# Performance work log

Measured on AMD Instinct MI355X. Metric: run time of the kernel, lower is better.

The kernel has to match this reference:

```python
import jax, jax.numpy as jnp
import numpy as np

HEAD_NUM = 8
DIM_QK = 64
DIM_V = 64
SPAN = 64
STRIDE = 4


def _sparse_indices(length_q, length_kv):
    # Replicates torch meshgrid index math (static, numpy).
    R = SPAN // STRIDE
    r = np.arange(R)[:, None]              # [R,1]
    c = np.arange(length_q)[None, :]       # [1,Lq]
    # ceil((c-(span-1))/stride) + r, via floor-div identity ceil(a/b) = -((-a)//b)
    qi_col = -((SPAN - 1 - c) // STRIDE) + r   # [R,Lq]
    qi_row = c - STRIDE * qi_col
    valid = (qi_row >= 0) & (qi_row < SPAN) & (qi_col >= 0) & (qi_col < length_kv)
    qc = np.clip(qi_col, 0, length_kv - 1)
    return jnp.asarray(qc, dtype=jnp.int32), jnp.asarray(valid)


def setup_inputs() -> dict:
    key = jax.random.key(0)
    ks = jax.random.split(key, 7)
    B, Lq, Lkv, D = 2, 4096, 1024, 512
    q = jax.random.normal(ks[0], (B, Lq, D), dtype=jnp.float32)
    k = jax.random.normal(ks[1], (B, Lkv, D), dtype=jnp.float32)
    v = jax.random.normal(ks[2], (B, Lkv, D), dtype=jnp.float32)
    Wq = jax.random.normal(ks[3], (D, HEAD_NUM * DIM_QK), dtype=jnp.float32) * 0.05
    Wk = jax.random.normal(ks[4], (D, HEAD_NUM * DIM_QK), dtype=jnp.float32) * 0.05
    Wv = jax.random.normal(ks[5], (D, HEAD_NUM * DIM_V), dtype=jnp.float32) * 0.05
    Wout = jax.random.normal(ks[6], (HEAD_NUM * DIM_V, D), dtype=jnp.float32) * 0.05
    return {"q": q, "k": k, "v": v, "Wq": Wq, "Wk": Wk, "Wv": Wv, "Wout": Wout}


def reference(q, k, v, Wq, Wk, Wv, Wout):
    B, Lq, _ = q.shape
    Lkv = k.shape[1]
    # Projections -> [B, H, L, D]
    Q = (q @ Wq).reshape(B, Lq, HEAD_NUM, DIM_QK).transpose(0, 2, 1, 3)
    K = (k @ Wk).reshape(B, Lkv, HEAD_NUM, DIM_QK).transpose(0, 2, 1, 3)
    V = (v @ Wv).reshape(B, Lkv, HEAD_NUM, DIM_V).transpose(0, 2, 1, 3)
    qc, valid = _sparse_indices(Lq, Lkv)          # [R,Lq]
    Kg = K[:, :, qc, :]                            # [B,H,R,Lq,DQK] gather
    scores = jnp.einsum("bhcd,bhrcd->bhrc", Q, Kg) / jnp.sqrt(jnp.float32(DIM_QK))
    big_neg = jnp.asarray(-1e30, scores.dtype)
    scores = jnp.where(valid[None, None], scores, big_neg)
    w = jax.nn.softmax(scores, axis=2)             # softmax over the R sparse slots
    w = jnp.where(valid[None, None], w, 0.0)
    Vg = V[:, :, qc, :]                            # [B,H,R,Lq,DV] gather
    ctx = jnp.einsum("bhrc,bhrcd->bhcd", w, Vg)   # [B,H,Lq,DV]
    ctx = ctx.transpose(0, 2, 1, 3).reshape(B, Lq, HEAD_NUM * DIM_V)
    return ctx @ Wout
```

## Files before the change

### kernel.cpp

```cpp
#include <hip/hip_runtime.h>
#include <math.h>

#define HN 8
#define DK 64
#define LQ 4096
#define LKV 1024
#define DMODEL 512
#define BATCH 2

typedef unsigned short u16;
typedef unsigned int u32;
typedef __attribute__((ext_vector_type(8))) __bf16 bf16x8;
typedef __attribute__((ext_vector_type(4))) float f32x4;
typedef __attribute__((ext_vector_type(8))) u16 u16x8;

__device__ __forceinline__ u16 f2bf(float f) {
    u32 u = __float_as_uint(f);
    u = u + 0x7fffu + ((u >> 16) & 1u);
    return (u16)(u >> 16);
}
__device__ __forceinline__ float bf2f(u16 u) {
    return __uint_as_float(((u32)u) << 16);
}

__device__ __forceinline__ void gl_lds16(const u16* g, u16* l) {
    __builtin_amdgcn_global_load_lds((const __attribute__((address_space(1))) u32*)g,
                                     (__attribute__((address_space(3))) u32*)l, 16, 0, 0);
}

template <bool BF16OUT>
__device__ __forceinline__ void gemm_body(const u16* __restrict__ A,
                                          const u16* __restrict__ Bt,
                                          void* __restrict__ Cp,
                                          int bx, int by) {
    __shared__ u16 As[128 * 32];
    __shared__ u16 Bs[64 * 32];

    const int tid = threadIdx.x;
    const int lane = tid & 63;
    const int wave = tid >> 6;
    const int wm = (wave >> 1) * 64;
    const int wn = (wave & 1) * 32;
    const int quad = lane >> 4;
    const int l16 = lane & 15;
    const size_t m0 = (size_t)by * 128;
    const size_t n0 = (size_t)bx * 64;

    f32x4 acc[4][2] = {};

    for (int k0 = 0; k0 < 512; k0 += 32) {
#pragma unroll
        for (int i = 0; i < 2; ++i) {
            const int id = i * 256 + tid;
            const int r = id >> 2;
            const int c = (id & 3) ^ ((r >> 1) & 3);
            gl_lds16(&A[(m0 + r) * 512 + k0 + c * 8], &As[(size_t)(i * 256 + wave * 64) * 8]);
        }
        {
            const int r = tid >> 2;
            const int c = (tid & 3) ^ ((r >> 1) & 3);
            gl_lds16(&Bt[(n0 + r) * 512 + k0 + c * 8], &Bs[(size_t)(wave * 64) * 8]);
        }
        __syncthreads();

        bf16x8 af[4], bfr[2];
#pragma unroll
        for (int i = 0; i < 4; ++i) {
            const int ra = wm + i * 16 + l16;
            const int ca = quad ^ ((ra >> 1) & 3);
            af[i] = *(const bf16x8*)&As[ra * 32 + ca * 8];
        }
#pragma unroll
        for (int j = 0; j < 2; ++j) {
            const int rb = wn + j * 16 + l16;
            const int cb = quad ^ ((rb >> 1) & 3);
            bfr[j] = *(const bf16x8*)&Bs[rb * 32 + cb * 8];
        }
#pragma unroll
        for (int i = 0; i < 4; ++i)
#pragma unroll
            for (int j = 0; j < 2; ++j)
                acc[i][j] = __builtin_amdgcn_mfma_f32_16x16x32_bf16(af[i], bfr[j], acc[i][j], 0, 0, 0);
        __syncthreads();
    }

#pragma unroll
    for (int i = 0; i < 4; ++i) {
#pragma unroll
        for (int j = 0; j < 2; ++j) {
            const size_t row = m0 + wm + i * 16 + quad * 4;
            const size_t col = n0 + wn + j * 16 + l16;
#pragma unroll
            for (int t = 0; t < 4; ++t) {
                if (BF16OUT)
                    ((u16*)Cp)[(row + t) * 512 + col] = f2bf(acc[i][j][t]);
                else
                    ((float*)Cp)[(row + t) * 512 + col] = acc[i][j][t];
            }
        }
    }
}

__global__ __launch_bounds__(256) void proj_fused(const u16* __restrict__ qb,
                                                  const u16* __restrict__ kb,
                                                  const u16* __restrict__ vb,
                                                  const u16* __restrict__ wqt,
                                                  const u16* __restrict__ wkt,
                                                  const u16* __restrict__ wvt,
                                                  u16* __restrict__ Qb,
                                                  u16* __restrict__ Kb,
                                                  u16* __restrict__ Vb) {
    const int idx = blockIdx.x;
    if (idx < 512)
        gemm_body<true>(qb, wqt, Qb, idx & 7, idx >> 3);
    else if (idx < 640)
        gemm_body<true>(kb, wkt, Kb, (idx - 512) & 7, (idx - 512) >> 3);
    else
        gemm_body<true>(vb, wvt, Vb, (idx - 640) & 7, (idx - 640) >> 3);
}

__global__ __launch_bounds__(256) void gemm_out(const u16* __restrict__ A,
                                                const u16* __restrict__ Bt,
                                                float* __restrict__ C) {
    gemm_body<false>(A, Bt, C, blockIdx.x & 7, blockIdx.x >> 3);
}

__global__ __launch_bounds__(256) void prep(const float* __restrict__ q,
                                            const float* __restrict__ k,
                                            const float* __restrict__ v,
                                            const float* __restrict__ Wq,
                                            const float* __restrict__ Wk,
                                            const float* __restrict__ Wv,
                                            const float* __restrict__ Wout,
                                            u16* __restrict__ qb, u16* __restrict__ kb,
                                            u16* __restrict__ vb,
                                            u16* __restrict__ wqt, u16* __restrict__ wkt,
                                            u16* __restrict__ wvt, u16* __restrict__ wot) {
    __shared__ float tbuf[32][33];
    const int bid = blockIdx.x;
    const int tid = threadIdx.x;

    if (bid < 3072) {
        const float* in;
        u16* outp;
        int i;
        if (bid < 2048)      { in = q; outp = qb; i = bid * 256 + tid; }
        else if (bid < 2560) { in = k; outp = kb; i = (bid - 2048) * 256 + tid; }
        else                 { in = v; outp = vb; i = (bid - 2560) * 256 + tid; }
        const float4 a = ((const float4*)in)[i * 2];
        const float4 b = ((const float4*)in)[i * 2 + 1];
        u16x8 r;
        r[0] = f2bf(a.x); r[1] = f2bf(a.y); r[2] = f2bf(a.z); r[3] = f2bf(a.w);
        r[4] = f2bf(b.x); r[5] = f2bf(b.y); r[6] = f2bf(b.z); r[7] = f2bf(b.w);
        *(u16x8*)&outp[(size_t)i * 8] = r;
    } else {
        const int wb = bid - 3072;
        const int z = wb >> 8;
        const int t = wb & 255;
        const float* W = (z == 0) ? Wq : (z == 1) ? Wk : (z == 2) ? Wv : Wout;
        u16* O = (z == 0) ? wqt : (z == 1) ? wkt : (z == 2) ? wvt : wot;
        const int tx = tid & 31;
        const int ty = tid >> 5;
        const int x = (t & 15) * 32 + tx;
        const int y0 = (t >> 4) * 32;
#pragma unroll
        for (int i = ty; i < 32; i += 8) tbuf[i][tx] = W[(size_t)(y0 + i) * 512 + x];
        __syncthreads();
#pragma unroll
        for (int i = ty; i < 32; i += 8)
            O[(size_t)((t & 15) * 32 + i) * 512 + y0 + tx] = f2bf(tbuf[tx][i]);
    }
}

__global__ __launch_bounds__(256) void attn_f32(const u16* __restrict__ Q,
                                                const u16* __restrict__ K,
                                                const u16* __restrict__ V,
                                                u16* __restrict__ ctx) {
    __shared__ float Ks[80][68];
    __shared__ float Vs[80][68];

    const int tid = threadIdx.x;
    const int c0 = blockIdx.x * 256;
    const int h = blockIdx.y;
    const int b = blockIdx.z;

    const int fd_c0 = (63 - c0) >> 2;
    const int win_lo = (fd_c0 < 0) ? -fd_c0 : 0;

    for (int i = tid; i < 80 * 8; i += 256) {
        int row = i >> 3;
        int d8 = i & 7;
        int col = win_lo + row;
        if (col < LKV) {
            size_t base = ((size_t)(b * LKV + col)) * DMODEL + h * DK + d8 * 8;
            u16x8 k8 = *(const u16x8*)&K[base];
            u16x8 v8 = *(const u16x8*)&V[base];
            float4 ka = make_float4(bf2f(k8[0]), bf2f(k8[1]), bf2f(k8[2]), bf2f(k8[3]));
            float4 kb4 = make_float4(bf2f(k8[4]), bf2f(k8[5]), bf2f(k8[6]), bf2f(k8[7]));
            float4 va = make_float4(bf2f(v8[0]), bf2f(v8[1]), bf2f(v8[2]), bf2f(v8[3]));
            float4 vb4 = make_float4(bf2f(v8[4]), bf2f(v8[5]), bf2f(v8[6]), bf2f(v8[7]));
            *(float4*)&Ks[row][d8 * 8] = ka;
            *(float4*)&Ks[row][d8 * 8 + 4] = kb4;
            *(float4*)&Vs[row][d8 * 8] = va;
            *(float4*)&Vs[row][d8 * 8 + 4] = vb4;
        }
    }
    __syncthreads();

    const int c = c0 + tid;
    const int fd = (63 - c) >> 2;

    float qreg[64];
    const u16* qp = &Q[((size_t)(b * LQ + c)) * DMODEL + h * DK];
#pragma unroll
    for (int i = 0; i < 8; ++i) {
        u16x8 t8 = *(const u16x8*)&qp[i * 8];
#pragma unroll
        for (int j = 0; j < 8; ++j) qreg[i * 8 + j] = bf2f(t8[j]);
    }

    float sc[16];
    float mx = -3.0e38f;
#pragma unroll
    for (int r = 0; r < 16; ++r) {
        int col = r - fd;
        if (col < 0) col = 0;
        const float* kr = &Ks[col - win_lo][0];
        float s = 0.f;
#pragma unroll
        for (int i = 0; i < 64; ++i) s = fmaf(qreg[i], kr[i], s);
        s *= 0.125f;
        sc[r] = (r >= fd) ? s : -1.0e30f;
        mx = fmaxf(mx, sc[r]);
    }

    float sum = 0.f;
#pragma unroll
    for (int r = 0; r < 16; ++r) {
        sc[r] = __expf(sc[r] - mx);
        sum += sc[r];
    }
    const float inv = 1.0f / sum;

    float acc[64];
#pragma unroll
    for (int i = 0; i < 64; ++i) acc[i] = 0.f;
#pragma unroll
    for (int r = 0; r < 16; ++r) {
        const float w = sc[r] * inv;
        int col = r - fd;
        if (col < 0) col = 0;
        const float* vr = &Vs[col - win_lo][0];
#pragma unroll
        for (int i = 0; i < 64; ++i) acc[i] = fmaf(w, vr[i], acc[i]);
    }

    u16* cp = &ctx[((size_t)(b * LQ + c)) * DMODEL + h * DK];
#pragma unroll
    for (int i = 0; i < 8; ++i) {
        u16x8 o;
#pragma unroll
        for (int j = 0; j < 8; ++j) o[j] = f2bf(acc[i * 8 + j]);
        *(u16x8*)&cp[i * 8] = o;
    }
}

extern "C" void kernel_launch(void* const* d_in, const int* in_sizes, int n_in,
                              void* d_out, int out_size, void* d_ws, size_t ws_size,
                              hipStream_t stream) {
    const float* q    = (const float*)d_in[0];
    const float* k    = (const float*)d_in[1];
    const float* v    = (const float*)d_in[2];
    const float* Wq   = (const float*)d_in[3];
    const float* Wk   = (const float*)d_in[4];
    const float* Wv   = (const float*)d_in[5];
    const float* Wout = (const float*)d_in[6];
    float* out = (float*)d_out;

    const size_t NQ = (size_t)BATCH * LQ * DMODEL;
    const size_t NK = (size_t)BATCH * LKV * DMODEL;
    const size_t NW = (size_t)DMODEL * DMODEL;

    u16* qb  = (u16*)d_ws;
    u16* kb  = qb + NQ;
    u16* vb  = kb + NK;
    u16* Qb  = vb + NK;
    u16* Kb  = Qb + NQ;
    u16* Vb  = Kb + NK;
    u16* cb  = Vb + NK;
    u16* wqt = cb + NQ;
    u16* wkt = wqt + NW;
    u16* wvt = wkt + NW;
    u16* wot = wvt + NW;

    prep<<<dim3(4096), dim3(256), 0, stream>>>(q, k, v, Wq, Wk, Wv, Wout,
                                               qb, kb, vb, wqt, wkt, wvt, wot);

    proj_fused<<<dim3(768), dim3(256), 0, stream>>>(qb, kb, vb, wqt, wkt, wvt, Qb, Kb, Vb);

    attn_f32<<<dim3(LQ / 256, HN, BATCH), dim3(256), 0, stream>>>(Qb, Kb, Vb, cb);

    gemm_out<<<dim3(512), dim3(256), 0, stream>>>(cb, wot, out);
}
```

Before: 135.3 us.

## Keep full weight panel resident in LDS and double-buffer A tiles in GEMMs

The projection and output GEMMs now load an entire 128x512 weight slice into shared memory once per block. They stream A tiles through a double buffer, prefetching the next tile before computing the current one, and use larger 128x128 output tiles with one barrier per k-step. The aim is to cut repeated weight reloads, halve the barriers, and overlap global loads with MFMA work. The attention kernel is also changed to 128-thread blocks with a smaller K/V window, giving more blocks. The cost is roughly 144KB of LDS per GEMM block, which allows only one block per CU and gives just 256 blocks, so occupancy and latency hiding suffer.

Result: no change. 133.4 us (-1.3%).

```diff
diff --git a/kernel.cpp b/kernel.cpp
--- a/kernel.cpp
+++ b/kernel.cpp
@@ -29,100 +29,122 @@
 }
 
 template <bool BF16OUT>
-__device__ __forceinline__ void gemm_body(const u16* __restrict__ A,
-                                          const u16* __restrict__ Bt,
-                                          void* __restrict__ Cp,
-                                          int bx, int by) {
-    __shared__ u16 As[128 * 32];
-    __shared__ u16 Bs[64 * 32];
-
+__device__ __forceinline__ void gemm_ws(const u16* __restrict__ A,
+                                        const u16* __restrict__ Bt,
+                                        void* __restrict__ Cp,
+                                        int m0base, int n0, int T,
+                                        u16* __restrict__ Bs,
+                                        u16* __restrict__ Asb) {
     const int tid = threadIdx.x;
     const int lane = tid & 63;
     const int wave = tid >> 6;
     const int wm = (wave >> 1) * 64;
-    const int wn = (wave & 1) * 32;
+    const int wn = (wave & 1) * 64;
     const int quad = lane >> 4;
     const int l16 = lane & 15;
-    const size_t m0 = (size_t)by * 128;
-    const size_t n0 = (size_t)bx * 64;
-
-    f32x4 acc[4][2] = {};
-
-    for (int k0 = 0; k0 < 512; k0 += 32) {
+
+#pragma unroll
+    for (int it = 0; it < 32; ++it) {
+        const int C = it * 256 + tid;
+        const int rb = C >> 6;
+        const int s = C & 63;
+        const int kc = (s & ~7) | ((s ^ rb) & 7);
+        gl_lds16(&Bt[(size_t)(n0 + rb) * 512 + kc * 8], &Bs[(size_t)(C & ~63) * 8]);
+    }
+
+    auto stageA = [&](int m0, int k0, int buf) {
 #pragma unroll
         for (int i = 0; i < 2; ++i) {
-            const int id = i * 256 + tid;
-            const int r = id >> 2;
-            const int c = (id & 3) ^ ((r >> 1) & 3);
-            gl_lds16(&A[(m0 + r) * 512 + k0 + c * 8], &As[(size_t)(i * 256 + wave * 64) * 8]);
+            const int C = i * 256 + tid;
+            const int r = C >> 2;
+            const int s = C & 3;
+            gl_lds16(&A[(size_t)(m0 + r) * 512 + k0 + s * 8],
+                     &Asb[(size_t)buf * 4096 + (size_t)(C & ~63) * 8]);
         }
-        {
-            const int r = tid >> 2;
-            const int c = (tid & 3) ^ ((r >> 1) & 3);
-            gl_lds16(&Bt[(n0 + r) * 512 + k0 + c * 8], &Bs[(size_t)(wave * 64) * 8]);
+    };
+
+    stageA(m0base, 0, 0);
+    int buf = 0;
+
+    for (int t = 0; t < T; ++t) {
+        const int m0 = m0base + t * 128;
+        f32x4 acc[4][4] = {};
+
+        for (int it = 0; it < 16; ++it) {
+            __syncthreads();
+            if (it < 15)
+                stageA(m0, (it + 1) * 32, buf ^ 1);
+            else if (t + 1 < T)
+                stageA(m0 + 128, 0, buf ^ 1);
+
+            bf16x8 af[4], bfr[4];
+#pragma unroll
+            for (int i = 0; i < 4; ++i) {
+                const int ra = wm + i * 16 + l16;
+                af[i] = *(const bf16x8*)&Asb[(size_t)buf * 4096 + (size_t)(ra * 4 + quad) * 8];
+            }
+#pragma unroll
+            for (int j = 0; j < 4; ++j) {
+                const int rb = wn + j * 16 + l16;
+                const int kc = it * 4 + quad;
+                const int slot = (kc & ~7) | ((kc ^ rb) & 7);
+                bfr[j] = *(const bf16x8*)&Bs[(size_t)(rb * 64 + slot) * 8];
+            }
+#pragma unroll
+            for (int i = 0; i < 4; ++i)
+#pragma unroll
+                for (int j = 0; j < 4; ++j)
+                    acc[i][j] = __builtin_amdgcn_mfma_f32_16x16x32_bf16(af[i], bfr[j], acc[i][j], 0, 0, 0);
+            buf ^= 1;
         }
-        __syncthreads();
-
-        bf16x8 af[4], bfr[2];
+
 #pragma unroll
         for (int i = 0; i < 4; ++i) {
-            const int ra = wm + i * 16 + l16;
-            const int ca = quad ^ ((ra >> 1) & 3);
-            af[i] = *(const bf16x8*)&As[ra * 32 + ca * 8];
-        }
-#pragma unroll
-        for (int j = 0; j < 2; ++j) {
-            const int rb = wn + j * 16 + l16;
-            const int cb = quad ^ ((rb >> 1) & 3);
-            bfr[j] = *(const bf16x8*)&Bs[rb * 32 + cb * 8];
-        }
-#pragma unroll
-        for (int i = 0; i < 4; ++i)
-#pragma unroll
-            for (int j = 0; j < 2; ++j)
-                acc[i][j] = __builtin_amdgcn_mfma_f32_16x16x32_bf16(af[i], bfr[j], acc[i][j], 0, 0, 0);
-        __syncthreads();
-    }
-
-#pragma unroll
-    for (int i = 0; i < 4; ++i) {
-#pragma unroll
-        for (int j = 0; j < 2; ++j) {
-            const size_t row = m0 + wm + i * 16 + quad * 4;
-            const size_t col = n0 + wn + j * 16 + l16;
-#pragma unroll
-            for (int t = 0; t < 4; ++t) {
-                if (BF16OUT)
-                    ((u16*)Cp)[(row + t) * 512 + col] = f2bf(acc[i][j][t]);
-                else
-                    ((float*)Cp)[(row + t) * 512 + col] = acc[i][j][t];
+#pragma unroll
+            for (int j = 0; j < 4; ++j) {
+                const size_t row = (size_t)m0 + wm + i * 16 + quad * 4;
+                const size_t col = (size_t)n0 + wn + j * 16 + l16;
+#pragma unroll
+                for (int u = 0; u < 4; ++u) {
+                    if (BF16OUT)
+                        ((u16*)Cp)[(row + u) * 512 + col] = f2bf(acc[i][j][u]);
+                    else
+                        ((float*)Cp)[(row + u) * 512 + col] = acc[i][j][u];
+                }
             }
         }
     }
 }
 
-__global__ __launch_bounds__(256) void proj_fused(const u16* __restrict__ qb,
-                                                  const u16* __restrict__ kb,
-                                                  const u16* __restrict__ vb,
-                                                  const u16* __restrict__ wqt,
-                                                  const u16* __restrict__ wkt,
-                                                  const u16* __restrict__ wvt,
-                                                  u16* __restrict__ Qb,
-                                                  u16* __restrict__ Kb,
-                                                  u16* __restrict__ Vb) {
+__global__ __launch_bounds__(256) void proj_ws(const u16* __restrict__ qb,
+                                               const u16* __restrict__ kb,
+                                               const u16* __restrict__ vb,
+                                               const u16* __restrict__ wqt,
+                                               const u16* __restrict__ wkt,
+                                               const u16* __restrict__ wvt,
+                                               u16* __restrict__ Qb,
+                                               u16* __restrict__ Kb,
+                                               u16* __restrict__ Vb) {
+    __shared__ u16 Bs[128 * 512];
+    __shared__ u16 Asb[2 * 128 * 32];
     const int idx = blockIdx.x;
-    if (idx < 512)
-        gemm_body<true>(qb, wqt, Qb, idx & 7, idx >> 3);
-    else if (idx < 640)
-        gemm_body<true>(kb, wkt, Kb, (idx - 512) & 7, (idx - 512) >> 3);
-    else
-        gemm_body<true>(vb, wvt, Vb, (idx - 640) & 7, (idx - 640) >> 3);
-}
-
-__global__ __launch_bounds__(256) void gemm_out(const u16* __restrict__ A,
-                                                const u16* __restrict__ Bt,
-                                                float* __restrict__ C) {
-    gemm_body<false>(A, Bt, C, blockIdx.x & 7, blockIdx.x >> 3);
+    if (idx < 128) {
+        gemm_ws<true>(qb, wqt, Qb, (idx >> 2) * 256, (idx & 3) * 128, 2, Bs, Asb);
+    } else if (idx < 192) {
+        const int j = idx - 128;
+        gemm_ws<true>(kb, wkt, Kb, (j >> 2) * 128, (j & 3) * 128, 1, Bs, Asb);
+    } else {
+        const int j = idx - 192;
+        gemm_ws<true>(vb, wvt, Vb, (j >> 2) * 128, (j & 3) * 128, 1, Bs, Asb);
+    }
+}
+
+__global__ __launch_bounds__(256) void out_ws(const u16* __restrict__ A,
+                                              const u16* __restrict__ Bt,
+                                              float* __restrict__ C) {
+    __shared__ u16 Bs[128 * 512];
+    __shared__ u16 Asb[2 * 128 * 32];
+    gemm_ws<false>(A, Bt, C, (blockIdx.x >> 2) * 128, (blockIdx.x & 3) * 128, 1, Bs, Asb);
 }
 
 __global__ __launch_bounds__(256) void prep(const float* __restrict__ q,
@@ -172,22 +194,22 @@
     }
 }
 
-__global__ __launch_bounds__(256) void attn_f32(const u16* __restrict__ Q,
+__global__ __launch_bounds__(128) void attn_f32(const u16* __restrict__ Q,
                                                 const u16* __restrict__ K,
                                                 const u16* __restrict__ V,
                                                 u16* __restrict__ ctx) {
-    __shared__ float Ks[80][68];
-    __shared__ float Vs[80][68];
+    __shared__ float Ks[48][68];
+    __shared__ float Vs[48][68];
 
     const int tid = threadIdx.x;
-    const int c0 = blockIdx.x * 256;
+    const int c0 = blockIdx.x * 128;
     const int h = blockIdx.y;
     const int b = blockIdx.z;
 
     const int fd_c0 = (63 - c0) >> 2;
     const int win_lo = (fd_c0 < 0) ? -fd_c0 : 0;
 
-    for (int i = tid; i < 80 * 8; i += 256) {
+    for (int i = tid; i < 48 * 8; i += 128) {
         int row = i >> 3;
         int d8 = i & 7;
         int col = win_lo + row;
@@ -195,14 +217,10 @@
             size_t base = ((size_t)(b * LKV + col)) * DMODEL + h * DK + d8 * 8;
             u16x8 k8 = *(const u16x8*)&K[base];
             u16x8 v8 = *(const u16x8*)&V[base];
-            float4 ka = make_float4(bf2f(k8[0]), bf2f(k8[1]), bf2f(k8[2]), bf2f(k8[3]));
-            float4 kb4 = make_float4(bf2f(k8[4]), bf2f(k8[5]), bf2f(k8[6]), bf2f(k8[7]));
-            float4 va = make_float4(bf2f(v8[0]), bf2f(v8[1]), bf2f(v8[2]), bf2f(v8[3]));
-            float4 vb4 = make_float4(bf2f(v8[4]), bf2f(v8[5]), bf2f(v8[6]), bf2f(v8[7]));
-            *(float4*)&Ks[row][d8 * 8] = ka;
-            *(float4*)&Ks[row][d8 * 8 + 4] = kb4;
-            *(float4*)&Vs[row][d8 * 8] = va;
-            *(float4*)&Vs[row][d8 * 8 + 4] = vb4;
+            *(float4*)&Ks[row][d8 * 8]     = make_float4(bf2f(k8[0]), bf2f(k8[1]), bf2f(k8[2]), bf2f(k8[3]));
+            *(float4*)&Ks[row][d8 * 8 + 4] = make_float4(bf2f(k8[4]), bf2f(k8[5]), bf2f(k8[6]), bf2f(k8[7]));
+            *(float4*)&Vs[row][d8 * 8]     = make_float4(bf2f(v8[0]), bf2f(v8[1]), bf2f(v8[2]), bf2f(v8[3]));
+            *(float4*)&Vs[row][d8 * 8 + 4] = make_float4(bf2f(v8[4]), bf2f(v8[5]), bf2f(v8[6]), bf2f(v8[7]));
         }
     }
     __syncthreads();
@@ -296,9 +314,9 @@
     prep<<<dim3(4096), dim3(256), 0, stream>>>(q, k, v, Wq, Wk, Wv, Wout,
                                                qb, kb, vb, wqt, wkt, wvt, wot);
 
-    proj_fused<<<dim3(768), dim3(256), 0, stream>>>(qb, kb, vb, wqt, wkt, wvt, Qb, Kb, Vb);
-
-    attn_f32<<<dim3(LQ / 256, HN, BATCH), dim3(256), 0, stream>>>(Qb, Kb, Vb, cb);
-
-    gemm_out<<<dim3(512), dim3(256), 0, stream>>>(cb, wot, out);
-}
+    proj_ws<<<dim3(256), dim3(256), 0, stream>>>(qb, kb, vb, wqt, wkt, wvt, Qb, Kb, Vb);
+
+    attn_f32<<<dim3(LQ / 128, HN, BATCH), dim3(128), 0, stream>>>(Qb, Kb, Vb, cb);
+
+    out_ws<<<dim3(256), dim3(256), 0, stream>>>(cb, wot, out);
+}
```
